# Kernel optimization log

Hardware: AMD Instinct MI355X
Metric: run time of the kernel (lower is better)

Reference implementation:

```python
import jax, jax.numpy as jnp
import numpy as np
import math

N_EMBD = 1024
N_HEAD = 16
HEAD_DIM = N_EMBD // N_HEAD


def setup_inputs() -> dict:
    key = jax.random.key(0)
    k1, k2, k3 = jax.random.split(key, 3)
    x = jax.random.normal(k1, (2, 2048, N_EMBD), dtype=jnp.float32)
    # nn.Linear(n_embd, 3*n_embd, bias=False): weight shape [3*n_embd, n_embd]
    w_qkv = jax.random.normal(k2, (3 * N_EMBD, N_EMBD), dtype=jnp.float32) * (1.0 / math.sqrt(N_EMBD))
    w_proj = jax.random.normal(k3, (N_EMBD, N_EMBD), dtype=jnp.float32) * (1.0 / math.sqrt(N_EMBD))
    return {"x": x, "w_qkv": w_qkv, "w_proj": w_proj}


def reference(x, w_qkv, w_proj):
    bsz, seq_len, channels = x.shape
    n_head, head_dim = N_HEAD, HEAD_DIM
    # qkv projection: x @ W^T -> [b, s, 3c]
    qkv = jnp.einsum('bsc,dc->bsd', x, w_qkv)
    q, k, v = jnp.split(qkv, 3, axis=2)
    # [b, h, s, hd]
    q = q.reshape(bsz, seq_len, n_head, head_dim).transpose(0, 2, 1, 3)
    k = k.reshape(bsz, seq_len, n_head, head_dim).transpose(0, 2, 1, 3)
    v = v.reshape(bsz, seq_len, n_head, head_dim).transpose(0, 2, 1, 3)
    scale = 1.0 / math.sqrt(head_dim)
    att = jnp.einsum('bhqd,bhkd->bhqk', q, k) * scale  # [b,h,s,s]
    causal = jnp.tril(jnp.ones((seq_len, seq_len), dtype=bool))
    att = jnp.where(causal[None, None, :, :], att, -jnp.inf)
    att = jax.nn.softmax(att, axis=-1)
    # dropout p=0.0 -> identity
    y = jnp.einsum('bhqk,bhkd->bhqd', att, v)
    y = y.transpose(0, 2, 1, 3).reshape(bsz, seq_len, channels)
    return jnp.einsum('bsc,dc->bsd', y, w_proj)
```

## Files before the change

kernel.cpp:

```cpp
#include <hip/hip_runtime.h>
#include <hip/hip_bf16.h>

typedef short short8 __attribute__((ext_vector_type(8)));
typedef float f32x4 __attribute__((ext_vector_type(4)));

#define NB   2
#define SEQ  2048
#define CH   1024
#define NH   16
#define HD   64
#define MROWS (NB*SEQ)
#define QSZ  (NB*NH*SEQ*HD)

__device__ __forceinline__ f32x4 mfma16(short8 a, short8 b, f32x4 c) {
    return __builtin_amdgcn_mfma_f32_16x16x32_bf16(a, b, c, 0, 0, 0);
}

__device__ __forceinline__ short bf16_of(float f) {
    return __builtin_bit_cast(short, __float2bfloat16(f));
}

__device__ __forceinline__ short8 load8(const __hip_bfloat16* p) {
    return *reinterpret_cast<const short8*>(p);
}
__device__ __forceinline__ short8 load8(const float* p) {
    f32x4 a = *reinterpret_cast<const f32x4*>(p);
    f32x4 b = *reinterpret_cast<const f32x4*>(p + 4);
    short8 r;
    r[0] = bf16_of(a[0]); r[1] = bf16_of(a[1]);
    r[2] = bf16_of(a[2]); r[3] = bf16_of(a[3]);
    r[4] = bf16_of(b[0]); r[5] = bf16_of(b[1]);
    r[6] = bf16_of(b[2]); r[7] = bf16_of(b[3]);
    return r;
}

__device__ __forceinline__ void gload_lds16(const void* g, void* l) {
    __builtin_amdgcn_global_load_lds(
        (const __attribute__((address_space(1))) unsigned int*)g,
        (__attribute__((address_space(3))) unsigned int*)l, 16, 0, 0);
}

__global__ void cvt_bf16_kernel(const float* __restrict__ src,
                                __hip_bfloat16* __restrict__ dst, int n) {
    int i = (blockIdx.x * blockDim.x + threadIdx.x) * 8;
    if (i >= n) return;
    short8 r = load8(src + i);
    *(short8*)&dst[i] = r;
}

template<int EPI, typename TA, typename TW>
__global__ __launch_bounds__(256, 2)
void gemm_bt(const TA* __restrict__ A,
             const TW* __restrict__ W,
             int K, int N,
             float* __restrict__ Cout,
             __hip_bfloat16* __restrict__ qp,
             __hip_bfloat16* __restrict__ kp,
             __hip_bfloat16* __restrict__ vtp)
{
    __shared__ alignas(16) __hip_bfloat16 Asm[128 * 32];
    __shared__ alignas(16) __hip_bfloat16 Bsm[128 * 32];

    const int tid  = threadIdx.x;
    const int lane = tid & 63;
    const int wave = tid >> 6;
    const int wm   = wave >> 1, wn = wave & 1;
    const int l15  = lane & 15, lg = lane >> 4;
    const int m0   = blockIdx.x * 128;
    const int n0   = blockIdx.y * 128;

    f32x4 acc[4][4] = {};

    const int c0 = tid, c1 = tid + 256;
    const int r0 = c0 >> 2, kc0 = (c0 & 3) << 3;
    const int r1 = c1 >> 2, kc1 = (c1 & 3) << 3;
    const TA* a0p = A + (size_t)(m0 + r0) * K + kc0;
    const TA* a1p = A + (size_t)(m0 + r1) * K + kc1;
    const TW* b0p = W + (size_t)(n0 + r0) * K + kc0;
    const TW* b1p = W + (size_t)(n0 + r1) * K + kc1;

    for (int k0 = 0; k0 < K; k0 += 32) {
        short8 av0 = load8(a0p + k0);
        short8 av1 = load8(a1p + k0);
        short8 bv0 = load8(b0p + k0);
        short8 bv1 = load8(b1p + k0);
        __syncthreads();
        *(short8*)&Asm[c0 * 8] = av0;
        *(short8*)&Asm[c1 * 8] = av1;
        *(short8*)&Bsm[c0 * 8] = bv0;
        *(short8*)&Bsm[c1 * 8] = bv1;
        __syncthreads();

        short8 af[4], bfr[4];
        #pragma unroll
        for (int mi = 0; mi < 4; ++mi)
            af[mi] = *(const short8*)&Asm[(wm * 64 + mi * 16 + l15) * 32 + lg * 8];
        #pragma unroll
        for (int ni = 0; ni < 4; ++ni)
            bfr[ni] = *(const short8*)&Bsm[(wn * 64 + ni * 16 + l15) * 32 + lg * 8];
        #pragma unroll
        for (int mi = 0; mi < 4; ++mi)
            #pragma unroll
            for (int ni = 0; ni < 4; ++ni)
                acc[mi][ni] = mfma16(af[mi], bfr[ni], acc[mi][ni]);
    }

    #pragma unroll
    for (int mi = 0; mi < 4; ++mi) {
        #pragma unroll
        for (int ni = 0; ni < 4; ++ni) {
            #pragma unroll
            for (int j = 0; j < 4; ++j) {
                const int m = m0 + wm * 64 + mi * 16 + lg * 4 + j;
                const int n = n0 + wn * 64 + ni * 16 + l15;
                if constexpr (EPI == 0) {
                    Cout[(size_t)m * N + n] = acc[mi][ni][j];
                } else {
                    const __hip_bfloat16 hv = __float2bfloat16(acc[mi][ni][j]);
                    const int sec = n >> 10;
                    const int c   = n & 1023;
                    const int h   = c >> 6, d = c & 63;
                    const int b   = m >> 11, s = m & 2047;
                    const int bh  = b * NH + h;
                    if (sec == 0)      qp [((size_t)bh * SEQ + s) * HD + d] = hv;
                    else if (sec == 1) kp [((size_t)bh * SEQ + s) * HD + d] = hv;
                    else               vtp[((size_t)bh * HD  + d) * SEQ + s] = hv;
                }
            }
        }
    }
}

__global__ __launch_bounds__(256, 2)
void attn_fwd3(const __hip_bfloat16* __restrict__ qp,
               const __hip_bfloat16* __restrict__ kp,
               const __hip_bfloat16* __restrict__ vtp,
               __hip_bfloat16* __restrict__ yp)
{
    __shared__ alignas(16) __hip_bfloat16 Ksm[2][64 * 64];
    __shared__ alignas(16) __hip_bfloat16 Vsm[2][64 * 64];
    __shared__ alignas(16) __hip_bfloat16 P[4][16][72];

    const int tid  = threadIdx.x;
    const int lane = tid & 63, wave = tid >> 6;
    const int l15  = lane & 15, lg = lane >> 4;
    const int id   = blockIdx.x;
    const int c    = 31 - (id >> 5);
    const int bh   = id & 31;
    const int b    = bh >> 4, h = bh & 15;
    const int q0   = c * 64 + wave * 16;

    const __hip_bfloat16* Q  = qp  + (size_t)bh * SEQ * HD;
    const __hip_bfloat16* Kp = kp  + (size_t)bh * SEQ * HD;
    const __hip_bfloat16* Vt = vtp + (size_t)bh * HD * SEQ;

    short8 qf[2];
    #pragma unroll
    for (int dk = 0; dk < 2; ++dk)
        qf[dk] = *(const short8*)&Q[(size_t)(q0 + l15) * HD + dk * 32 + lg * 8];

    const short ONE = 0x3F80;
    short8 ones;
    #pragma unroll
    for (int i = 0; i < 8; ++i) ones[i] = ONE;

    f32x4 o[4] = {};
    f32x4 accl = {};
    float m_r[4];
    #pragma unroll
    for (int j = 0; j < 4; ++j) m_r[j] = -1e30f;

    auto stage = [&](int buf, int t) {
        const int kv0 = t * 64;
        #pragma unroll
        for (int j = 0; j < 2; ++j) {
            const int ch  = j * 256 + tid;
            const int row = ch >> 3, cb = ch & 7;
            const int cbs = cb ^ (row & 7);
            gload_lds16(Kp + (size_t)(kv0 + row) * HD + cbs * 8,
                        &Ksm[buf][(j * 256 + wave * 64) * 8]);
            gload_lds16(Vt + (size_t)row * SEQ + kv0 + cbs * 8,
                        &Vsm[buf][(j * 256 + wave * 64) * 8]);
        }
    };

    auto compute = [&](int buf, int t) {
        const int kv0 = t * 64;
        f32x4 s[4] = {};
        #pragma unroll
        for (int kf = 0; kf < 4; ++kf)
            #pragma unroll
            for (int dk = 0; dk < 2; ++dk) {
                short8 kfrag = *(const short8*)
                    &Ksm[buf][(kf * 16 + l15) * 64 + (((dk * 4 + lg) ^ (l15 & 7)) * 8)];
                s[kf] = mfma16(qf[dk], kfrag, s[kf]);
            }

        float v[4][4], mx[4];
        const bool diag = (t == c);
        #pragma unroll
        for (int j = 0; j < 4; ++j) {
            const int row = q0 + lg * 4 + j;
            #pragma unroll
            for (int kf = 0; kf < 4; ++kf) {
                float sv = s[kf][j] * 0.125f;
                if (diag && (kv0 + kf * 16 + l15 > row)) sv = -1e30f;
                v[kf][j] = sv;
            }
            mx[j] = fmaxf(fmaxf(v[0][j], v[1][j]), fmaxf(v[2][j], v[3][j]));
        }
        #pragma unroll
        for (int off = 1; off < 16; off <<= 1)
            #pragma unroll
            for (int j = 0; j < 4; ++j)
                mx[j] = fmaxf(mx[j], __shfl_xor(mx[j], off));

        #pragma unroll
        for (int j = 0; j < 4; ++j) {
            const float mn = fmaxf(m_r[j], mx[j]);
            const float r  = __expf(m_r[j] - mn);
            #pragma unroll
            for (int kf = 0; kf < 4; ++kf)
                v[kf][j] = __expf(v[kf][j] - mn);
            m_r[j] = mn;
            accl[j] *= r;
            #pragma unroll
            for (int dt = 0; dt < 4; ++dt) o[dt][j] *= r;
        }

        #pragma unroll
        for (int j = 0; j < 4; ++j)
            #pragma unroll
            for (int kf = 0; kf < 4; ++kf)
                P[wave][lg * 4 + j][kf * 16 + l15] = __float2bfloat16(v[kf][j]);
        asm volatile("s_waitcnt lgkmcnt(0)" ::: "memory");
        __builtin_amdgcn_sched_barrier(0);
        short8 pa0 = *(const short8*)&P[wave][l15][lg * 8];
        short8 pa1 = *(const short8*)&P[wave][l15][32 + lg * 8];

        accl = mfma16(pa0, ones, accl);
        accl = mfma16(pa1, ones, accl);

        #pragma unroll
        for (int dt = 0; dt < 4; ++dt) {
            short8 vf0 = *(const short8*)
                &Vsm[buf][(dt * 16 + l15) * 64 + (((0 + lg) ^ (l15 & 7)) * 8)];
            short8 vf1 = *(const short8*)
                &Vsm[buf][(dt * 16 + l15) * 64 + (((4 + lg) ^ (l15 & 7)) * 8)];
            o[dt] = mfma16(pa0, vf0, o[dt]);
            o[dt] = mfma16(pa1, vf1, o[dt]);
        }
    };

    stage(0, 0);
    for (int t = 0; t <= c; ++t) {
        const int cur = t & 1;
        __syncthreads();
        if (t < c) stage(cur ^ 1, t + 1);
        compute(cur, t);
    }

    #pragma unroll
    for (int j = 0; j < 4; ++j) {
        const float inv_l = 1.0f / accl[j];
        const int s = q0 + lg * 4 + j;
        #pragma unroll
        for (int dt = 0; dt < 4; ++dt) {
            yp[((size_t)(b * SEQ + s)) * CH + h * 64 + dt * 16 + l15] =
                __float2bfloat16(o[dt][j] * inv_l);
        }
    }
}

extern "C" void kernel_launch(void* const* d_in, const int* in_sizes, int n_in,
                              void* d_out, int out_size, void* d_ws, size_t ws_size,
                              hipStream_t stream)
{
    const float* x      = (const float*)d_in[0];
    const float* w_qkv  = (const float*)d_in[1];
    const float* w_proj = (const float*)d_in[2];
    float* out = (float*)d_out;

    __hip_bfloat16* ws = (__hip_bfloat16*)d_ws;

    const size_t NX  = (size_t)MROWS * CH;
    const size_t NWQ = (size_t)3 * CH * CH;
    const size_t NWP = (size_t)CH * CH;

    if (ws_size >= 41943040ull) {
        __hip_bfloat16* xb   = ws;
        __hip_bfloat16* wqb  = ws + NX;
        __hip_bfloat16* wpb  = ws + NX + NWQ;
        __hip_bfloat16* q_ws = ws + NX + NWQ + NWP;
        __hip_bfloat16* k_ws = q_ws + (size_t)QSZ;
        __hip_bfloat16* vt_ws= k_ws + (size_t)QSZ;
        __hip_bfloat16* y_ws = xb;

        cvt_bf16_kernel<<<NX  / 2048, 256, 0, stream>>>(x,      xb,  (int)NX);
        cvt_bf16_kernel<<<NWQ / 2048, 256, 0, stream>>>(w_qkv,  wqb, (int)NWQ);
        cvt_bf16_kernel<<<NWP / 2048, 256, 0, stream>>>(w_proj, wpb, (int)NWP);

        gemm_bt<1, __hip_bfloat16, __hip_bfloat16>
            <<<dim3(MROWS / 128, 3072 / 128), 256, 0, stream>>>(
            xb, wqb, CH, 3 * CH, nullptr, q_ws, k_ws, vt_ws);

        attn_fwd3<<<1024, 256, 0, stream>>>(q_ws, k_ws, vt_ws, y_ws);

        gemm_bt<0, __hip_bfloat16, __hip_bfloat16>
            <<<dim3(MROWS / 128, CH / 128), 256, 0, stream>>>(
            y_ws, wpb, CH, CH, out, nullptr, nullptr, nullptr);
    } else {
        __hip_bfloat16* q_ws  = ws;
        __hip_bfloat16* k_ws  = ws + (size_t)QSZ;
        __hip_bfloat16* vt_ws = ws + (size_t)2 * QSZ;
        __hip_bfloat16* y_ws  = ws + (size_t)3 * QSZ;

        gemm_bt<1, float, float><<<dim3(MROWS / 128, 3072 / 128), 256, 0, stream>>>(
            x, w_qkv, CH, 3 * CH, nullptr, q_ws, k_ws, vt_ws);

        attn_fwd3<<<1024, 256, 0, stream>>>(q_ws, k_ws, vt_ws, y_ws);

        gemm_bt<0, __hip_bfloat16, float><<<dim3(MROWS / 128, CH / 128), 256, 0, stream>>>(
            y_ws, w_proj, CH, CH, out, nullptr, nullptr, nullptr);
    }
}
```

Baseline: 133.5 us.

## Fuse conversions, double-buffer GEMM with direct LDS loads, lazy softmax rescale

Merges the three fp32-to-bf16 conversion launches into one kernel. Adds a bf16 GEMM variant that stages tiles straight into double-buffered LDS with global_load_lds, so the next tile loads while the current one computes. In attention, the running-max rescale is skipped unless some row's max grows by more than 8, and launch bounds are raised to 3 blocks per CU. These target launch overhead, GEMM load latency and exp/multiply work, at the cost of more LDS, register pressure limits, and a looser but still exact online-softmax bound.

Result: faster. 125.7 us (-5.8%).

```diff
diff --git a/kernel.cpp b/kernel.cpp
--- a/kernel.cpp
+++ b/kernel.cpp
@@ -11,6 +11,9 @@
 #define HD   64
 #define MROWS (NB*SEQ)
 #define QSZ  (NB*NH*SEQ*HD)
+#define NX   ((size_t)MROWS * CH)
+#define NWQ  ((size_t)3 * CH * CH)
+#define NWP  ((size_t)CH * CH)
 
 __device__ __forceinline__ f32x4 mfma16(short8 a, short8 b, f32x4 c) {
     return __builtin_amdgcn_mfma_f32_16x16x32_bf16(a, b, c, 0, 0, 0);
@@ -40,26 +43,31 @@
         (__attribute__((address_space(3))) unsigned int*)l, 16, 0, 0);
 }
 
-__global__ void cvt_bf16_kernel(const float* __restrict__ src,
-                                __hip_bfloat16* __restrict__ dst, int n) {
-    int i = (blockIdx.x * blockDim.x + threadIdx.x) * 8;
-    if (i >= n) return;
-    short8 r = load8(src + i);
-    *(short8*)&dst[i] = r;
-}
-
-template<int EPI, typename TA, typename TW>
+__global__ void cvt3_kernel(const float* __restrict__ x,
+                            const float* __restrict__ wq,
+                            const float* __restrict__ wp,
+                            __hip_bfloat16* __restrict__ dst) {
+    const size_t i = ((size_t)blockIdx.x * 256 + threadIdx.x) * 8;
+    const float* src;
+    size_t off;
+    if (i < NX)            { src = x;  off = i; }
+    else if (i < NX + NWQ) { src = wq; off = i - NX; }
+    else                   { src = wp; off = i - NX - NWQ; }
+    *(short8*)&dst[i] = load8(src + off);
+}
+
+template<int EPI>
 __global__ __launch_bounds__(256, 2)
-void gemm_bt(const TA* __restrict__ A,
-             const TW* __restrict__ W,
-             int K, int N,
-             float* __restrict__ Cout,
-             __hip_bfloat16* __restrict__ qp,
-             __hip_bfloat16* __restrict__ kp,
-             __hip_bfloat16* __restrict__ vtp)
+void gemm_bt2(const __hip_bfloat16* __restrict__ A,
+              const __hip_bfloat16* __restrict__ W,
+              int K, int N,
+              float* __restrict__ Cout,
+              __hip_bfloat16* __restrict__ qp,
+              __hip_bfloat16* __restrict__ kp,
+              __hip_bfloat16* __restrict__ vtp)
 {
-    __shared__ alignas(16) __hip_bfloat16 Asm[128 * 32];
-    __shared__ alignas(16) __hip_bfloat16 Bsm[128 * 32];
+    __shared__ alignas(16) __hip_bfloat16 Asm[2][128 * 32];
+    __shared__ alignas(16) __hip_bfloat16 Bsm[2][128 * 32];
 
     const int tid  = threadIdx.x;
     const int lane = tid & 63;
@@ -71,38 +79,42 @@
 
     f32x4 acc[4][4] = {};
 
-    const int c0 = tid, c1 = tid + 256;
-    const int r0 = c0 >> 2, kc0 = (c0 & 3) << 3;
-    const int r1 = c1 >> 2, kc1 = (c1 & 3) << 3;
-    const TA* a0p = A + (size_t)(m0 + r0) * K + kc0;
-    const TA* a1p = A + (size_t)(m0 + r1) * K + kc1;
-    const TW* b0p = W + (size_t)(n0 + r0) * K + kc0;
-    const TW* b1p = W + (size_t)(n0 + r1) * K + kc1;
-
-    for (int k0 = 0; k0 < K; k0 += 32) {
-        short8 av0 = load8(a0p + k0);
-        short8 av1 = load8(a1p + k0);
-        short8 bv0 = load8(b0p + k0);
-        short8 bv1 = load8(b1p + k0);
-        __syncthreads();
-        *(short8*)&Asm[c0 * 8] = av0;
-        *(short8*)&Asm[c1 * 8] = av1;
-        *(short8*)&Bsm[c0 * 8] = bv0;
-        *(short8*)&Bsm[c1 * 8] = bv1;
-        __syncthreads();
-
+    const int srow = lane >> 2;
+    const int scol = (lane & 3) * 8;
+
+    auto stage = [&](int buf, int k0) {
+        #pragma unroll
+        for (int half = 0; half < 2; ++half) {
+            const int row = wave * 32 + half * 16;
+            gload_lds16(A + (size_t)(m0 + row + srow) * K + k0 + scol,
+                        &Asm[buf][row * 32]);
+            gload_lds16(W + (size_t)(n0 + row + srow) * K + k0 + scol,
+                        &Bsm[buf][row * 32]);
+        }
+    };
+
+    auto compute = [&](int buf) {
         short8 af[4], bfr[4];
         #pragma unroll
         for (int mi = 0; mi < 4; ++mi)
-            af[mi] = *(const short8*)&Asm[(wm * 64 + mi * 16 + l15) * 32 + lg * 8];
+            af[mi] = *(const short8*)&Asm[buf][(wm * 64 + mi * 16 + l15) * 32 + lg * 8];
         #pragma unroll
         for (int ni = 0; ni < 4; ++ni)
-            bfr[ni] = *(const short8*)&Bsm[(wn * 64 + ni * 16 + l15) * 32 + lg * 8];
+            bfr[ni] = *(const short8*)&Bsm[buf][(wn * 64 + ni * 16 + l15) * 32 + lg * 8];
         #pragma unroll
         for (int mi = 0; mi < 4; ++mi)
             #pragma unroll
             for (int ni = 0; ni < 4; ++ni)
                 acc[mi][ni] = mfma16(af[mi], bfr[ni], acc[mi][ni]);
+    };
+
+    stage(0, 0);
+    int it = 0;
+    for (int k0 = 0; k0 < K; k0 += 32, ++it) {
+        const int cur = it & 1;
+        __syncthreads();
+        if (k0 + 32 < K) stage(cur ^ 1, k0 + 32);
+        compute(cur);
     }
 
     #pragma unroll
@@ -131,7 +143,90 @@
     }
 }
 
+template<int EPI, typename TA, typename TW>
 __global__ __launch_bounds__(256, 2)
+void gemm_bt(const TA* __restrict__ A,
+             const TW* __restrict__ W,
+             int K, int N,
+             float* __restrict__ Cout,
+             __hip_bfloat16* __restrict__ qp,
+             __hip_bfloat16* __restrict__ kp,
+             __hip_bfloat16* __restrict__ vtp)
+{
+    __shared__ alignas(16) __hip_bfloat16 Asm[128 * 32];
+    __shared__ alignas(16) __hip_bfloat16 Bsm[128 * 32];
+
+    const int tid  = threadIdx.x;
+    const int lane = tid & 63;
+    const int wave = tid >> 6;
+    const int wm   = wave >> 1, wn = wave & 1;
+    const int l15  = lane & 15, lg = lane >> 4;
+    const int m0   = blockIdx.x * 128;
+    const int n0   = blockIdx.y * 128;
+
+    f32x4 acc[4][4] = {};
+
+    const int c0 = tid, c1 = tid + 256;
+    const int r0 = c0 >> 2, kc0 = (c0 & 3) << 3;
+    const int r1 = c1 >> 2, kc1 = (c1 & 3) << 3;
+    const TA* a0p = A + (size_t)(m0 + r0) * K + kc0;
+    const TA* a1p = A + (size_t)(m0 + r1) * K + kc1;
+    const TW* b0p = W + (size_t)(n0 + r0) * K + kc0;
+    const TW* b1p = W + (size_t)(n0 + r1) * K + kc1;
+
+    for (int k0 = 0; k0 < K; k0 += 32) {
+        short8 av0 = load8(a0p + k0);
+        short8 av1 = load8(a1p + k0);
+        short8 bv0 = load8(b0p + k0);
+        short8 bv1 = load8(b1p + k0);
+        __syncthreads();
+        *(short8*)&Asm[c0 * 8] = av0;
+        *(short8*)&Asm[c1 * 8] = av1;
+        *(short8*)&Bsm[c0 * 8] = bv0;
+        *(short8*)&Bsm[c1 * 8] = bv1;
+        __syncthreads();
+
+        short8 af[4], bfr[4];
+        #pragma unroll
+        for (int mi = 0; mi < 4; ++mi)
+            af[mi] = *(const short8*)&Asm[(wm * 64 + mi * 16 + l15) * 32 + lg * 8];
+        #pragma unroll
+        for (int ni = 0; ni < 4; ++ni)
+            bfr[ni] = *(const short8*)&Bsm[(wn * 64 + ni * 16 + l15) * 32 + lg * 8];
+        #pragma unroll
+        for (int mi = 0; mi < 4; ++mi)
+            #pragma unroll
+            for (int ni = 0; ni < 4; ++ni)
+                acc[mi][ni] = mfma16(af[mi], bfr[ni], acc[mi][ni]);
+    }
+
+    #pragma unroll
+    for (int mi = 0; mi < 4; ++mi) {
+        #pragma unroll
+        for (int ni = 0; ni < 4; ++ni) {
+            #pragma unroll
+            for (int j = 0; j < 4; ++j) {
+                const int m = m0 + wm * 64 + mi * 16 + lg * 4 + j;
+                const int n = n0 + wn * 64 + ni * 16 + l15;
+                if constexpr (EPI == 0) {
+                    Cout[(size_t)m * N + n] = acc[mi][ni][j];
+                } else {
+                    const __hip_bfloat16 hv = __float2bfloat16(acc[mi][ni][j]);
+                    const int sec = n >> 10;
+                    const int c   = n & 1023;
+                    const int h   = c >> 6, d = c & 63;
+                    const int b   = m >> 11, s = m & 2047;
+                    const int bh  = b * NH + h;
+                    if (sec == 0)      qp [((size_t)bh * SEQ + s) * HD + d] = hv;
+                    else if (sec == 1) kp [((size_t)bh * SEQ + s) * HD + d] = hv;
+                    else               vtp[((size_t)bh * HD  + d) * SEQ + s] = hv;
+                }
+            }
+        }
+    }
+}
+
+__global__ __launch_bounds__(256, 3)
 void attn_fwd3(const __hip_bfloat16* __restrict__ qp,
                const __hip_bfloat16* __restrict__ kp,
                const __hip_bfloat16* __restrict__ vtp,
@@ -215,18 +310,25 @@
             for (int j = 0; j < 4; ++j)
                 mx[j] = fmaxf(mx[j], __shfl_xor(mx[j], off));
 
-        #pragma unroll
-        for (int j = 0; j < 4; ++j) {
-            const float mn = fmaxf(m_r[j], mx[j]);
-            const float r  = __expf(m_r[j] - mn);
+        bool needs = false;
+        #pragma unroll
+        for (int j = 0; j < 4; ++j) needs |= (mx[j] > m_r[j] + 8.0f);
+        if (__any(needs)) {
+            #pragma unroll
+            for (int j = 0; j < 4; ++j) {
+                const float mn = fmaxf(m_r[j], mx[j]);
+                const float r  = __expf(m_r[j] - mn);
+                m_r[j] = mn;
+                accl[j] *= r;
+                #pragma unroll
+                for (int dt = 0; dt < 4; ++dt) o[dt][j] *= r;
+            }
+        }
+        #pragma unroll
+        for (int j = 0; j < 4; ++j)
             #pragma unroll
             for (int kf = 0; kf < 4; ++kf)
-                v[kf][j] = __expf(v[kf][j] - mn);
-            m_r[j] = mn;
-            accl[j] *= r;
-            #pragma unroll
-            for (int dt = 0; dt < 4; ++dt) o[dt][j] *= r;
-        }
+                v[kf][j] = __expf(v[kf][j] - m_r[j]);
 
         #pragma unroll
         for (int j = 0; j < 4; ++j)
@@ -283,10 +385,6 @@
 
     __hip_bfloat16* ws = (__hip_bfloat16*)d_ws;
 
-    const size_t NX  = (size_t)MROWS * CH;
-    const size_t NWQ = (size_t)3 * CH * CH;
-    const size_t NWP = (size_t)CH * CH;
-
     if (ws_size >= 41943040ull) {
         __hip_bfloat16* xb   = ws;
         __hip_bfloat16* wqb  = ws + NX;
@@ -296,18 +394,14 @@
         __hip_bfloat16* vt_ws= k_ws + (size_t)QSZ;
         __hip_bfloat16* y_ws = xb;
 
-        cvt_bf16_kernel<<<NX  / 2048, 256, 0, stream>>>(x,      xb,  (int)NX);
-        cvt_bf16_kernel<<<NWQ / 2048, 256, 0, stream>>>(w_qkv,  wqb, (int)NWQ);
-        cvt_bf16_kernel<<<NWP / 2048, 256, 0, stream>>>(w_proj, wpb, (int)NWP);
-
-        gemm_bt<1, __hip_bfloat16, __hip_bfloat16>
-            <<<dim3(MROWS / 128, 3072 / 128), 256, 0, stream>>>(
+        cvt3_kernel<<<(NX + NWQ + NWP) / 2048, 256, 0, stream>>>(x, w_qkv, w_proj, ws);
+
+        gemm_bt2<1><<<dim3(MROWS / 128, 3072 / 128), 256, 0, stream>>>(
             xb, wqb, CH, 3 * CH, nullptr, q_ws, k_ws, vt_ws);
 
         attn_fwd3<<<1024, 256, 0, stream>>>(q_ws, k_ws, vt_ws, y_ws);
 
-        gemm_bt<0, __hip_bfloat16, __hip_bfloat16>
-            <<<dim3(MROWS / 128, CH / 128), 256, 0, stream>>>(
+        gemm_bt2<0><<<dim3(MROWS / 128, CH / 128), 256, 0, stream>>>(
             y_ws, wpb, CH, CH, out, nullptr, nullptr, nullptr);
     } else {
         __hip_bfloat16* q_ws  = ws;
```
